# Performance work log

Measured on AMD Instinct MI355X. Metric: run time of the kernel, lower is better.

The kernel has to match this reference:

```python
import jax, jax.numpy as jnp
import numpy as np

NUM_HEADS = 12
NUM_TASKS = 4


def setup_inputs() -> dict:
    key = jax.random.key(0)
    k1, k2, k3, k4 = jax.random.split(key, 4)
    B, N, C = 2, 2048, 768
    x = jax.random.normal(k1, (B, N, C), dtype=jnp.float32)
    # nn.Linear(dim, 3*dim, bias=False): store as [C, 3C] so y = x @ w_qkv
    w_qkv = jax.random.normal(k2, (C, 3 * C), dtype=jnp.float32) * (C ** -0.5)
    w_proj = jax.random.normal(k3, (C, C), dtype=jnp.float32) * (C ** -0.5)
    b_proj = jax.random.normal(k4, (C,), dtype=jnp.float32) * 0.01
    return {"x": x, "w_qkv": w_qkv, "w_proj": w_proj, "b_proj": b_proj}


def reference(x, w_qkv, w_proj, b_proj):
    B, N, C = x.shape
    H = NUM_HEADS
    d = C // H
    scale = d ** -0.5
    qkv = (x @ w_qkv).reshape(B, N, 3, H, d)
    qkv = jnp.transpose(qkv, (2, 0, 3, 1, 4))  # [3, B, H, N, d]
    q, k, v = qkv[0], qkv[1], qkv[2]
    attn = jnp.einsum("bhnd,bhmd->bhnm", q, k) * scale
    attn = jax.nn.softmax(attn, axis=-1)
    # static task mask: zero cross-task attention among first NUM_TASKS tokens
    mask = jnp.ones((N, N), dtype=attn.dtype).at[:NUM_TASKS, :NUM_TASKS].set(
        jnp.eye(NUM_TASKS, dtype=attn.dtype))
    attn = attn * mask  # broadcasts over [B, H, N, N]
    out = jnp.einsum("bhnm,bhmd->bhnd", attn, v)
    out = jnp.transpose(out, (0, 2, 1, 3)).reshape(B, N, C)
    return out @ w_proj + b_proj
```

## Files before the change

### kernel.cpp

```cpp
#include <hip/hip_runtime.h>

typedef __attribute__((ext_vector_type(4))) float f32x4;
typedef __attribute__((ext_vector_type(8))) __bf16 bf16x8;
typedef __attribute__((ext_vector_type(4))) __bf16 bf16x4;

#define QSCALE (0.125f * 1.4426950408889634f)

__device__ __forceinline__ void load_lds16(const void* g, void* l) {
  __builtin_amdgcn_global_load_lds(
      (const __attribute__((address_space(1))) unsigned int*)g,
      (__attribute__((address_space(3))) unsigned int*)l, 16, 0, 0);
}

__device__ __forceinline__ f32x4 mfma16(bf16x8 a, bf16x8 b, f32x4 c) {
  return __builtin_amdgcn_mfma_f32_16x16x32_bf16(a, b, c, 0, 0, 0);
}

__device__ __forceinline__ bf16x8 cat44(bf16x4 a, bf16x4 b) {
  return __builtin_shufflevector(a, b, 0, 1, 2, 3, 4, 5, 6, 7);
}


__global__ __launch_bounds__(256) void k_cast_x(const float* __restrict__ in,
                                                __bf16* __restrict__ out) {
  int i = blockIdx.x * 256 + threadIdx.x;
  const f32x4* in4 = (const f32x4*)in;
  f32x4 a = in4[i * 2], b = in4[i * 2 + 1];
  bf16x8 o;
  o[0] = (__bf16)a[0]; o[1] = (__bf16)a[1]; o[2] = (__bf16)a[2]; o[3] = (__bf16)a[3];
  o[4] = (__bf16)b[0]; o[5] = (__bf16)b[1]; o[6] = (__bf16)b[2]; o[7] = (__bf16)b[3];
  *(bf16x8*)(out + (size_t)i * 8) = o;
}

__global__ void k_transpose_cast(const float* __restrict__ in, __bf16* __restrict__ out,
                                 int R, int C) {
  __shared__ float t[32][33];
  int c0 = blockIdx.x * 32, r0 = blockIdx.y * 32;
  int tx = threadIdx.x, ty = threadIdx.y;
#pragma unroll
  for (int j = 0; j < 32; j += 8)
    t[ty + j][tx] = in[(size_t)(r0 + ty + j) * C + c0 + tx];
  __syncthreads();
#pragma unroll
  for (int j = 0; j < 32; j += 8)
    out[(size_t)(c0 + ty + j) * R + r0 + tx] = (__bf16)t[tx][ty + j];
}


template <int NT>
__device__ __forceinline__ void gemm_core(const char* aB, const char* bB,
                                          char* smem, int tid, int l,
                                          int wr, int wc, f32x4 (&acc)[4][4]) {
  auto stage = [&](int buf, int kt) {
#pragma unroll
    for (int is = 0; is < 2; ++is) {
      int o = is * 4096 + tid * 16;
      int row = o >> 6, cb = (o >> 4) & 3;
      int src = row * 1536 + (((cb ^ row) & 3) << 4) + kt * 64;
      load_lds16(aB + src, smem + buf * 8192 + o);
      load_lds16(bB + src, smem + 16384 + buf * 8192 + o);
    }
  };
  stage(0, 0);
#pragma unroll 2
  for (int kt = 0; kt < NT; ++kt) {
    int cur = kt & 1;
    __syncthreads();
    if (kt + 1 < NT) stage(cur ^ 1, kt + 1);
    const __bf16* As = (const __bf16*)(smem + cur * 8192);
    const __bf16* Bs = (const __bf16*)(smem + 16384 + cur * 8192);
    bf16x8 af[4], bfr[4];
#pragma unroll
    for (int mf = 0; mf < 4; ++mf) {
      int row = wr * 64 + mf * 16 + (l & 15);
      af[mf] = *(const bf16x8*)&As[row * 32 + ((((l >> 4) ^ row) & 3) << 3)];
    }
#pragma unroll
    for (int nf = 0; nf < 4; ++nf) {
      int row = wc * 64 + nf * 16 + (l & 15);
      bfr[nf] = *(const bf16x8*)&Bs[row * 32 + ((((l >> 4) ^ row) & 3) << 3)];
    }
    __builtin_amdgcn_s_setprio(1);
#pragma unroll
    for (int mf = 0; mf < 4; ++mf)
#pragma unroll
      for (int nf = 0; nf < 4; ++nf)
        acc[mf][nf] = mfma16(af[mf], bfr[nf], acc[mf][nf]);
    __builtin_amdgcn_s_setprio(0);
  }
  __syncthreads();
}


__global__ __launch_bounds__(256, 3) void k_qkv(const __bf16* __restrict__ A,
                                                const __bf16* __restrict__ BT,
                                                __bf16* __restrict__ qb,
                                                __bf16* __restrict__ kb,
                                                __bf16* __restrict__ vT) {
  __shared__ __align__(16) char smem[32768];
  int tid = threadIdx.x, l = tid & 63, w = tid >> 6, wr = w >> 1, wc = w & 1;
  int g = l >> 4, c = l & 15;
  int m0 = blockIdx.y * 128, n0 = blockIdx.x * 128;
  f32x4 acc[4][4] = {};
  gemm_core<24>((const char*)(A + (size_t)m0 * 768), (const char*)(BT + (size_t)n0 * 768),
                smem, tid, l, wr, wc, acc);
  int b = m0 >> 11, m0l = m0 & 2047;
  int sel = n0 / 768;
  int rem = n0 - sel * 768;

  if (sel == 2) {
#pragma unroll
    for (int mf = 0; mf < 4; ++mf) {
      int tokb = wr * 64 + mf * 16 + 4 * g;
      int gr = tokb >> 3, low = (g & 1) << 3;
#pragma unroll
      for (int nf = 0; nf < 4; ++nf) {
        int dd = wc * 64 + nf * 16 + c;
        bf16x4 pk;
        pk[0] = (__bf16)acc[mf][nf][0]; pk[1] = (__bf16)acc[mf][nf][1];
        pk[2] = (__bf16)acc[mf][nf][2]; pk[3] = (__bf16)acc[mf][nf][3];
        *(bf16x4*)(smem + dd * 256 + (((gr ^ (dd & 15)) & 15) << 4) + low) = pk;
      }
    }
    __syncthreads();
#pragma unroll
    for (int p = 0; p < 8; ++p) {
      int idx = p * 256 + tid;
      int dd = idx >> 4, t8 = idx & 15;
      bf16x8 v = *(const bf16x8*)(smem + dd * 256 + (((t8 ^ (dd & 15)) & 15) << 4));
      int colg = rem + dd;
      int h = colg >> 6, d = colg & 63;
      *(bf16x8*)(vT + (((size_t)(b * 12 + h)) * 64 + d) * 2048 + m0l + t8 * 8) = v;
    }
  } else {
    float qs = (sel == 0) ? QSCALE : 1.0f;
#pragma unroll
    for (int mf = 0; mf < 4; ++mf)
#pragma unroll
      for (int nf = 0; nf < 4; ++nf) {
        int col = wc * 64 + nf * 16 + c;
        int grc = col >> 3, lowc = (col & 7) << 1;
#pragma unroll
        for (int r = 0; r < 4; ++r) {
          int tok = wr * 64 + mf * 16 + 4 * g + r;
          *(__bf16*)(smem + tok * 256 + (((grc ^ (tok & 15)) & 15) << 4) + lowc) =
              (__bf16)(acc[mf][nf][r] * qs);
        }
      }
    __syncthreads();
    __bf16* dst0 = (sel == 0) ? qb : kb;
#pragma unroll
    for (int p = 0; p < 8; ++p) {
      int idx = p * 256 + tid;
      int tok = idx >> 4, hh = (idx >> 3) & 1, d8 = idx & 7;
      int gr = hh * 8 + d8;
      bf16x8 v = *(const bf16x8*)(smem + tok * 256 + (((gr ^ (tok & 15)) & 15) << 4));
      int h = (rem >> 6) + hh;
      *(bf16x8*)(dst0 + (((size_t)(b * 12 + h)) * 2048 + m0l + tok) * 64 + d8 * 8) = v;
    }
  }
}


__global__ __launch_bounds__(256, 4) void k_attn(const __bf16* __restrict__ qb,
                                                 const __bf16* __restrict__ kb,
                                                 const __bf16* __restrict__ vT,
                                                 __bf16* __restrict__ Op01,
                                                 __bf16* __restrict__ Op23,
                                                 float* __restrict__ lpart) {
  __shared__ __align__(16) char smem[32768];
  int tid = threadIdx.x, l = tid & 63, w = tid >> 6;
  int g = l >> 4, c = l & 15;
  int phys = blockIdx.x;
  int lid = (phys & 7) * 192 + (phys >> 3);
  int qt = lid & 15;
  int bhsp = lid >> 4;
  int bh = bhsp % 24, sp = bhsp / 24;

  const char* qbase  = (const char*)qb + ((size_t)bh * 2048 + qt * 128) * 128;
  const char* kbase0 = (const char*)kb + (size_t)bh * 262144 + (size_t)sp * 65536;
  const char* vbase0 = (const char*)vT + (size_t)bh * 262144 + sp * 1024;

#pragma unroll
  for (int is = 0; is < 4; ++is) {
    int o = is * 4096 + tid * 16;
    int row = o >> 7, cb = (o >> 4) & 7;
    load_lds16(qbase + row * 128 + (((cb ^ row) & 7) << 4), smem + o);
  }
  __syncthreads();
  bf16x8 qf[2][2];
#pragma unroll
  for (int qi = 0; qi < 2; ++qi)
#pragma unroll
    for (int ks = 0; ks < 2; ++ks) {
      int q = w * 32 + qi * 16 + c;
      int gg = ks * 4 + g;
      qf[qi][ks] = *(const bf16x8*)(smem + q * 128 + (((gg ^ q) & 7) << 3) * 2);
    }
  __syncthreads();

  auto stageKV = [&](int buf, int t) {
    const char* kbase = kbase0 + t * 8192;
    const char* vbase = vbase0 + t * 128;
#pragma unroll
    for (int is = 0; is < 2; ++is) {
      int o = is * 4096 + tid * 16;
      int r = o >> 7, cb = (o >> 4) & 7;
      load_lds16(kbase + r * 128 + (((cb ^ r) & 7) << 4), smem + buf * 8192 + o);
      load_lds16(vbase + (size_t)r * 4096 + (((cb ^ r) & 7) << 4),
                 smem + 16384 + buf * 8192 + o);
    }
  };

  float lacc[2] = {0.f, 0.f};
  f32x4 accO[2][4] = {};

  stageKV(0, 0);
#pragma unroll 2
  for (int t = 0; t < 8; ++t) {
    int cur = t & 1;
    __syncthreads();
    if (t + 1 < 8) stageKV(cur ^ 1, t + 1);
    const char* KsB = smem + cur * 8192;
    const char* VsB = smem + 16384 + cur * 8192;

    f32x4 s[4][2];
#pragma unroll
    for (int kf = 0; kf < 4; ++kf) {
      s[kf][0] = f32x4{0.f, 0.f, 0.f, 0.f};
      s[kf][1] = f32x4{0.f, 0.f, 0.f, 0.f};
    }
    __builtin_amdgcn_s_setprio(1);
#pragma unroll
    for (int ks = 0; ks < 2; ++ks) {
#pragma unroll
      for (int kf = 0; kf < 4; ++kf) {
        int key = kf * 16 + c;
        int gg = ks * 4 + g;
        bf16x8 kfr = *(const bf16x8*)(KsB + key * 128 + (((gg ^ key) & 7) << 4));
        s[kf][0] = mfma16(kfr, qf[0][ks], s[kf][0]);
        s[kf][1] = mfma16(kfr, qf[1][ks], s[kf][1]);
      }
    }
    __builtin_amdgcn_s_setprio(0);

#pragma unroll
    for (int kf = 0; kf < 4; ++kf)
#pragma unroll
      for (int qi = 0; qi < 2; ++qi)
#pragma unroll
        for (int r = 0; r < 4; ++r) {
          float p = __builtin_amdgcn_exp2f(s[kf][qi][r]);
          s[kf][qi][r] = p;
          lacc[qi] += p;
        }

    if (sp == 0 && qt == 0 && t == 0 && w == 0 && g == 0 && c < 4) {
#pragma unroll
      for (int r = 0; r < 4; ++r)
        if (r != c) s[0][0][r] = 0.f;
    }

    bf16x4 pkv[2][4];
#pragma unroll
    for (int qi = 0; qi < 2; ++qi)
#pragma unroll
      for (int kf = 0; kf < 4; ++kf) {
        bf16x4 pk;
        pk[0] = (__bf16)s[kf][qi][0]; pk[1] = (__bf16)s[kf][qi][1];
        pk[2] = (__bf16)s[kf][qi][2]; pk[3] = (__bf16)s[kf][qi][3];
        pkv[qi][kf] = pk;
      }

    __builtin_amdgcn_s_setprio(1);
#pragma unroll
    for (int ks = 0; ks < 2; ++ks) {
      bf16x8 pa0 = cat44(pkv[0][2 * ks], pkv[0][2 * ks + 1]);
      bf16x8 pa1 = cat44(pkv[1][2 * ks], pkv[1][2 * ks + 1]);
      int low = (g & 1) << 3;
      int vc0 = ks * 4 + (g >> 1);
#pragma unroll
      for (int df = 0; df < 4; ++df) {
        int dd = df * 16 + c;
        const char* vrow = VsB + dd * 128;
        bf16x4 v0 = *(const bf16x4*)(vrow + (((vc0 ^ dd) & 7) << 4) + low);
        bf16x4 v1 = *(const bf16x4*)(vrow + ((((vc0 + 2) ^ dd) & 7) << 4) + low);
        bf16x8 vb = cat44(v0, v1);
        accO[0][df] = mfma16(pa0, vb, accO[0][df]);
        accO[1][df] = mfma16(pa1, vb, accO[1][df]);
      }
    }
    __builtin_amdgcn_s_setprio(0);
  }
  __syncthreads();

  size_t pbase = ((size_t)(sp & 1) * 24 + bh) * 2048 + qt * 128;
  __bf16* Obase = (sp < 2) ? Op01 : Op23;
  float lfull[2];
#pragma unroll
  for (int qi = 0; qi < 2; ++qi) {
    float rr = lacc[qi];
    rr += __shfl_xor(rr, 16, 64);
    rr += __shfl_xor(rr, 32, 64);
    lfull[qi] = rr;
  }
  if (g == 0) {
    size_t lb = ((size_t)sp * 24 + bh) * 2048 + qt * 128;
#pragma unroll
    for (int qi = 0; qi < 2; ++qi)
      lpart[lb + w * 32 + qi * 16 + c] = lfull[qi];
  }

  char* ep = smem + w * 4096;
#pragma unroll
  for (int mf = 0; mf < 2; ++mf) {
#pragma unroll
    for (int df = 0; df < 4; ++df) {
      int col = df * 16 + c;
      int sI = col >> 2, lowc = (col & 3) << 2;
#pragma unroll
      for (int r = 0; r < 4; ++r) {
        int rloc = 4 * g + r;
        *(float*)(ep + rloc * 256 + (((sI ^ rloc) & 15) << 4) + lowc) = accO[mf][df][r];
      }
    }
    int rr = l >> 2, q4 = l & 3;
    f32x4 aa[4];
#pragma unroll
    for (int j = 0; j < 4; ++j) {
      int sj = q4 * 4 + j;
      aa[j] = *(const f32x4*)(ep + rr * 256 + (((sj ^ rr) & 15) << 4));
    }
    bf16x8 o0, o1;
#pragma unroll
    for (int j = 0; j < 4; ++j) { o0[j] = (__bf16)aa[0][j]; o0[4 + j] = (__bf16)aa[1][j]; }
#pragma unroll
    for (int j = 0; j < 4; ++j) { o1[j] = (__bf16)aa[2][j]; o1[4 + j] = (__bf16)aa[3][j]; }
    int q = w * 32 + mf * 16 + rr;
    char* dst = (char*)Obase + (pbase + q) * 128 + q4 * 32;
    *(bf16x8*)dst = o0;
    *(bf16x8*)(dst + 16) = o1;
  }
}


__global__ __launch_bounds__(256) void k_combine(const __bf16* __restrict__ Op01,
                                                 const __bf16* __restrict__ Op23,
                                                 const float* __restrict__ lpart,
                                                 __bf16* __restrict__ ao) {
  int i = blockIdx.x * 256 + threadIdx.x;
  int d8 = i & 7, q = (i >> 3) & 2047, bh = i >> 14;
  int bg = bh / 12, h = bh - bg * 12;
  const size_t SPL = 24ull * 2048 * 64;
  size_t o0 = (((size_t)bh) * 2048 + q) * 64 + d8 * 8;
  bf16x8 a = *(const bf16x8*)(Op01 + o0);
  bf16x8 b = *(const bf16x8*)(Op01 + SPL + o0);
  bf16x8 cc = *(const bf16x8*)(Op23 + o0);
  bf16x8 d = *(const bf16x8*)(Op23 + SPL + o0);
  size_t lq = (size_t)bh * 2048 + q;
  float lsum = lpart[lq] + lpart[24ull * 2048 + lq] +
               lpart[2 * 24ull * 2048 + lq] + lpart[3 * 24ull * 2048 + lq];
  float rl = __builtin_amdgcn_rcpf(lsum);
  bf16x8 o;
#pragma unroll
  for (int j = 0; j < 8; ++j)
    o[j] = (__bf16)(((float)a[j] + (float)b[j] + (float)cc[j] + (float)d[j]) * rl);
  *(bf16x8*)(ao + ((size_t)bg * 2048 + q) * 768 + h * 64 + d8 * 8) = o;
}


__global__ __launch_bounds__(256, 3) void k_proj(const __bf16* __restrict__ A,
                                                 const __bf16* __restrict__ BT,
                                                 const float* __restrict__ bias,
                                                 float* __restrict__ out) {
  __shared__ __align__(16) char smem[32768];
  int tid = threadIdx.x, l = tid & 63, w = tid >> 6, wr = w >> 1, wc = w & 1;
  int m0 = blockIdx.y * 128, n0 = blockIdx.x * 128;
  f32x4 acc[4][4] = {};
  gemm_core<24>((const char*)(A + (size_t)m0 * 768), (const char*)(BT + (size_t)n0 * 768),
                smem, tid, l, wr, wc, acc);
#pragma unroll
  for (int nf = 0; nf < 4; ++nf) {
    int cc = n0 + wc * 64 + nf * 16 + (l & 15);
    float bi = bias[cc];
#pragma unroll
    for (int mf = 0; mf < 4; ++mf) {
      int m = m0 + wr * 64 + mf * 16 + ((l >> 4) << 2);
#pragma unroll
      for (int r = 0; r < 4; ++r)
        out[(size_t)(m + r) * 768 + cc] = acc[mf][nf][r] + bi;
    }
  }
}


extern "C" void kernel_launch(void* const* d_in, const int* in_sizes, int n_in,
                              void* d_out, int out_size, void* d_ws, size_t ws_size,
                              hipStream_t stream) {
  const float* x      = (const float*)d_in[0];
  const float* w_qkv  = (const float*)d_in[1];
  const float* w_proj = (const float*)d_in[2];
  const float* b_proj = (const float*)d_in[3];
  float* out = (float*)d_out;

  char* ws = (char*)d_ws;
  size_t off = 0;
  auto alloc = [&](size_t bytes) {
    char* p = ws + off;
    off += (bytes + 255) & ~(size_t)255;
    return p;
  };
  __bf16* xb     = (__bf16*)alloc(4096ull * 768 * 2);
  __bf16* wqkvT  = (__bf16*)alloc(2304ull * 768 * 2);
  __bf16* wprojT = (__bf16*)alloc(768ull * 768 * 2);
  __bf16* qb     = (__bf16*)alloc(24ull * 2048 * 64 * 2);
  __bf16* kb     = (__bf16*)alloc(24ull * 2048 * 64 * 2);
  __bf16* vT     = (__bf16*)alloc(24ull * 64 * 2048 * 2);
  __bf16* ao     = (__bf16*)alloc(4096ull * 768 * 2);
  __bf16* Op01   = (__bf16*)alloc(2ull * 24 * 2048 * 64 * 2);
  float*  lpart  = (float*)alloc(4ull * 24 * 2048 * 4);
  __bf16* Op23   = (__bf16*)d_out;

  k_cast_x<<<1536, 256, 0, stream>>>(x, xb);
  k_transpose_cast<<<dim3(72, 24), dim3(32, 8), 0, stream>>>(w_qkv, wqkvT, 768, 2304);
  k_transpose_cast<<<dim3(24, 24), dim3(32, 8), 0, stream>>>(w_proj, wprojT, 768, 768);
  k_qkv<<<dim3(18, 32), 256, 0, stream>>>(xb, wqkvT, qb, kb, vT);
  k_attn<<<1536, 256, 0, stream>>>(qb, kb, vT, Op01, Op23, lpart);
  k_combine<<<1536, 256, 0, stream>>>(Op01, Op23, lpart, ao);
  k_proj<<<dim3(6, 32), 256, 0, stream>>>(ao, wprojT, b_proj, out);
}
```

Baseline: 104.0 us.

## Triple-buffer GEMM and attention pipelines and halve attention KV split count

Replaces double-buffered LDS staging in the GEMM core and the attention kernel with a three-stage ring. Waits use explicit vmcnt waits plus raw barriers so two tiles stay in flight while one is computed. The attention split-K drops from 4 to 2 partitions, giving 768 blocks that each process 16 KV tiles, and the combine kernel now reads half the partial outputs. LDS per block grows to 48KB, which may reduce occupancy. Fewer attention blocks may also lower parallelism.

```diff
diff --git a/kernel.cpp b/kernel.cpp
--- a/kernel.cpp
+++ b/kernel.cpp
@@ -5,6 +5,13 @@
 typedef __attribute__((ext_vector_type(4))) __bf16 bf16x4;
 
 #define QSCALE (0.125f * 1.4426950408889634f)
+
+#define WAITV4 do { asm volatile("s_waitcnt vmcnt(4)" ::: "memory"); \
+  __builtin_amdgcn_sched_barrier(0); __builtin_amdgcn_s_barrier(); \
+  __builtin_amdgcn_sched_barrier(0); } while (0)
+#define WAITV0 do { asm volatile("s_waitcnt vmcnt(0)" ::: "memory"); \
+  __builtin_amdgcn_sched_barrier(0); __builtin_amdgcn_s_barrier(); \
+  __builtin_amdgcn_sched_barrier(0); } while (0)
 
 __device__ __forceinline__ void load_lds16(const void* g, void* l) {
   __builtin_amdgcn_global_load_lds(
@@ -47,10 +54,9 @@
 }
 
 
-template <int NT>
-__device__ __forceinline__ void gemm_core(const char* aB, const char* bB,
-                                          char* smem, int tid, int l,
-                                          int wr, int wc, f32x4 (&acc)[4][4]) {
+__device__ __forceinline__ void gemm_core24(const char* aB, const char* bB,
+                                            char* smem, int tid, int l,
+                                            int wr, int wc, f32x4 (&acc)[4][4]) {
   auto stage = [&](int buf, int kt) {
 #pragma unroll
     for (int is = 0; is < 2; ++is) {
@@ -58,17 +64,12 @@
       int row = o >> 6, cb = (o >> 4) & 3;
       int src = row * 1536 + (((cb ^ row) & 3) << 4) + kt * 64;
       load_lds16(aB + src, smem + buf * 8192 + o);
-      load_lds16(bB + src, smem + 16384 + buf * 8192 + o);
+      load_lds16(bB + src, smem + 24576 + buf * 8192 + o);
     }
   };
-  stage(0, 0);
-#pragma unroll 2
-  for (int kt = 0; kt < NT; ++kt) {
-    int cur = kt & 1;
-    __syncthreads();
-    if (kt + 1 < NT) stage(cur ^ 1, kt + 1);
-    const __bf16* As = (const __bf16*)(smem + cur * 8192);
-    const __bf16* Bs = (const __bf16*)(smem + 16384 + cur * 8192);
+  auto compute = [&](int buf) {
+    const __bf16* As = (const __bf16*)(smem + buf * 8192);
+    const __bf16* Bs = (const __bf16*)(smem + 24576 + buf * 8192);
     bf16x8 af[4], bfr[4];
 #pragma unroll
     for (int mf = 0; mf < 4; ++mf) {
@@ -87,7 +88,17 @@
       for (int nf = 0; nf < 4; ++nf)
         acc[mf][nf] = mfma16(af[mf], bfr[nf], acc[mf][nf]);
     __builtin_amdgcn_s_setprio(0);
-  }
+  };
+  stage(0, 0); stage(1, 1);
+#pragma unroll 3
+  for (int t = 0; t < 21; ++t) {
+    WAITV4;
+    stage((t + 2) % 3, t + 2);
+    compute(t % 3);
+  }
+  WAITV4; stage(2, 23); compute(0);
+  WAITV4; compute(1);
+  WAITV0; compute(2);
   __syncthreads();
 }
 
@@ -97,13 +108,13 @@
                                                 __bf16* __restrict__ qb,
                                                 __bf16* __restrict__ kb,
                                                 __bf16* __restrict__ vT) {
-  __shared__ __align__(16) char smem[32768];
+  __shared__ __align__(16) char smem[49152];
   int tid = threadIdx.x, l = tid & 63, w = tid >> 6, wr = w >> 1, wc = w & 1;
   int g = l >> 4, c = l & 15;
   int m0 = blockIdx.y * 128, n0 = blockIdx.x * 128;
   f32x4 acc[4][4] = {};
-  gemm_core<24>((const char*)(A + (size_t)m0 * 768), (const char*)(BT + (size_t)n0 * 768),
-                smem, tid, l, wr, wc, acc);
+  gemm_core24((const char*)(A + (size_t)m0 * 768), (const char*)(BT + (size_t)n0 * 768),
+              smem, tid, l, wr, wc, acc);
   int b = m0 >> 11, m0l = m0 & 2047;
   int sel = n0 / 768;
   int rem = n0 - sel * 768;
@@ -165,21 +176,20 @@
 __global__ __launch_bounds__(256, 4) void k_attn(const __bf16* __restrict__ qb,
                                                  const __bf16* __restrict__ kb,
                                                  const __bf16* __restrict__ vT,
-                                                 __bf16* __restrict__ Op01,
-                                                 __bf16* __restrict__ Op23,
+                                                 __bf16* __restrict__ Opart,
                                                  float* __restrict__ lpart) {
-  __shared__ __align__(16) char smem[32768];
+  __shared__ __align__(16) char smem[49152];
   int tid = threadIdx.x, l = tid & 63, w = tid >> 6;
   int g = l >> 4, c = l & 15;
   int phys = blockIdx.x;
-  int lid = (phys & 7) * 192 + (phys >> 3);
+  int lid = (phys & 7) * 96 + (phys >> 3);
   int qt = lid & 15;
   int bhsp = lid >> 4;
   int bh = bhsp % 24, sp = bhsp / 24;
 
   const char* qbase  = (const char*)qb + ((size_t)bh * 2048 + qt * 128) * 128;
-  const char* kbase0 = (const char*)kb + (size_t)bh * 262144 + (size_t)sp * 65536;
-  const char* vbase0 = (const char*)vT + (size_t)bh * 262144 + sp * 1024;
+  const char* kbase0 = (const char*)kb + (size_t)bh * 262144 + (size_t)sp * 131072;
+  const char* vbase0 = (const char*)vT + (size_t)bh * 262144 + sp * 2048;
 
 #pragma unroll
   for (int is = 0; is < 4; ++is) {
@@ -195,7 +205,7 @@
     for (int ks = 0; ks < 2; ++ks) {
       int q = w * 32 + qi * 16 + c;
       int gg = ks * 4 + g;
-      qf[qi][ks] = *(const bf16x8*)(smem + q * 128 + (((gg ^ q) & 7) << 3) * 2);
+      qf[qi][ks] = *(const bf16x8*)(smem + q * 128 + (((gg ^ q) & 7) << 4));
     }
   __syncthreads();
 
@@ -208,22 +218,16 @@
       int r = o >> 7, cb = (o >> 4) & 7;
       load_lds16(kbase + r * 128 + (((cb ^ r) & 7) << 4), smem + buf * 8192 + o);
       load_lds16(vbase + (size_t)r * 4096 + (((cb ^ r) & 7) << 4),
-                 smem + 16384 + buf * 8192 + o);
+                 smem + 24576 + buf * 8192 + o);
     }
   };
 
   float lacc[2] = {0.f, 0.f};
   f32x4 accO[2][4] = {};
 
-  stageKV(0, 0);
-#pragma unroll 2
-  for (int t = 0; t < 8; ++t) {
-    int cur = t & 1;
-    __syncthreads();
-    if (t + 1 < 8) stageKV(cur ^ 1, t + 1);
-    const char* KsB = smem + cur * 8192;
-    const char* VsB = smem + 16384 + cur * 8192;
-
+  auto compute = [&](int t, int buf) {
+    const char* KsB = smem + buf * 8192;
+    const char* VsB = smem + 24576 + buf * 8192;
     f32x4 s[4][2];
 #pragma unroll
     for (int kf = 0; kf < 4; ++kf) {
@@ -291,11 +295,22 @@
       }
     }
     __builtin_amdgcn_s_setprio(0);
-  }
+  };
+
+  stageKV(0, 0); stageKV(1, 1);
+#pragma unroll 3
+  for (int t = 0; t < 12; ++t) {
+    WAITV4;
+    stageKV((t + 2) % 3, t + 2);
+    compute(t, t % 3);
+  }
+  WAITV4; stageKV(2, 14); compute(12, 0);
+  WAITV4; stageKV(0, 15); compute(13, 1);
+  WAITV4; compute(14, 2);
+  WAITV0; compute(15, 0);
   __syncthreads();
 
-  size_t pbase = ((size_t)(sp & 1) * 24 + bh) * 2048 + qt * 128;
-  __bf16* Obase = (sp < 2) ? Op01 : Op23;
+  size_t pbase = ((size_t)sp * 24 + bh) * 2048 + qt * 128;
   float lfull[2];
 #pragma unroll
   for (int qi = 0; qi < 2; ++qi) {
@@ -305,10 +320,9 @@
     lfull[qi] = rr;
   }
   if (g == 0) {
-    size_t lb = ((size_t)sp * 24 + bh) * 2048 + qt * 128;
 #pragma unroll
     for (int qi = 0; qi < 2; ++qi)
-      lpart[lb + w * 32 + qi * 16 + c] = lfull[qi];
+      lpart[pbase + w * 32 + qi * 16 + c] = lfull[qi];
   }
 
   char* ep = smem + w * 4096;
@@ -324,6 +338,7 @@
         *(float*)(ep + rloc * 256 + (((sI ^ rloc) & 15) << 4) + lowc) = accO[mf][df][r];
       }
     }
+    asm volatile("s_waitcnt lgkmcnt(0)" ::: "memory");
     int rr = l >> 2, q4 = l & 3;
     f32x4 aa[4];
 #pragma unroll
@@ -337,15 +352,14 @@
 #pragma unroll
     for (int j = 0; j < 4; ++j) { o1[j] = (__bf16)aa[2][j]; o1[4 + j] = (__bf16)aa[3][j]; }
     int q = w * 32 + mf * 16 + rr;
-    char* dst = (char*)Obase + (pbase + q) * 128 + q4 * 32;
+    char* dst = (char*)Opart + (pbase + q) * 128 + q4 * 32;
     *(bf16x8*)dst = o0;
     *(bf16x8*)(dst + 16) = o1;
   }
 }
 
 
-__global__ __launch_bounds__(256) void k_combine(const __bf16* __restrict__ Op01,
-                                                 const __bf16* __restrict__ Op23,
+__global__ __launch_bounds__(256) void k_combine(const __bf16* __restrict__ Opart,
                                                  const float* __restrict__ lpart,
                                                  __bf16* __restrict__ ao) {
   int i = blockIdx.x * 256 + threadIdx.x;
@@ -353,18 +367,15 @@
   int bg = bh / 12, h = bh - bg * 12;
   const size_t SPL = 24ull * 2048 * 64;
   size_t o0 = (((size_t)bh) * 2048 + q) * 64 + d8 * 8;
-  bf16x8 a = *(const bf16x8*)(Op01 + o0);
-  bf16x8 b = *(const bf16x8*)(Op01 + SPL + o0);
-  bf16x8 cc = *(const bf16x8*)(Op23 + o0);
-  bf16x8 d = *(const bf16x8*)(Op23 + SPL + o0);
+  bf16x8 a = *(const bf16x8*)(Opart + o0);
+  bf16x8 b = *(const bf16x8*)(Opart + SPL + o0);
   size_t lq = (size_t)bh * 2048 + q;
-  float lsum = lpart[lq] + lpart[24ull * 2048 + lq] +
-               lpart[2 * 24ull * 2048 + lq] + lpart[3 * 24ull * 2048 + lq];
+  float lsum = lpart[lq] + lpart[24ull * 2048 + lq];
   float rl = __builtin_amdgcn_rcpf(lsum);
   bf16x8 o;
 #pragma unroll
   for (int j = 0; j < 8; ++j)
-    o[j] = (__bf16)(((float)a[j] + (float)b[j] + (float)cc[j] + (float)d[j]) * rl);
+    o[j] = (__bf16)(((float)a[j] + (float)b[j]) * rl);
   *(bf16x8*)(ao + ((size_t)bg * 2048 + q) * 768 + h * 64 + d8 * 8) = o;
 }
 
@@ -373,12 +384,12 @@
                                                  const __bf16* __restrict__ BT,
                                                  const float* __restrict__ bias,
                                                  float* __restrict__ out) {
-  __shared__ __align__(16) char smem[32768];
+  __shared__ __align__(16) char smem[49152];
   int tid = threadIdx.x, l = tid & 63, w = tid >> 6, wr = w >> 1, wc = w & 1;
   int m0 = blockIdx.y * 128, n0 = blockIdx.x * 128;
   f32x4 acc[4][4] = {};
-  gemm_core<24>((const char*)(A + (size_t)m0 * 768), (const char*)(BT + (size_t)n0 * 768),
-                smem, tid, l, wr, wc, acc);
+  gemm_core24((const char*)(A + (size_t)m0 * 768), (const char*)(BT + (size_t)n0 * 768),
+              smem, tid, l, wr, wc, acc);
 #pragma unroll
   for (int nf = 0; nf < 4; ++nf) {
     int cc = n0 + wc * 64 + nf * 16 + (l & 15);
@@ -417,15 +428,14 @@
   __bf16* kb     = (__bf16*)alloc(24ull * 2048 * 64 * 2);
   __bf16* vT     = (__bf16*)alloc(24ull * 64 * 2048 * 2);
   __bf16* ao     = (__bf16*)alloc(4096ull * 768 * 2);
-  __bf16* Op01   = (__bf16*)alloc(2ull * 24 * 2048 * 64 * 2);
-  float*  lpart  = (float*)alloc(4ull * 24 * 2048 * 4);
-  __bf16* Op23   = (__bf16*)d_out;
+  __bf16* Opart  = (__bf16*)alloc(2ull * 24 * 2048 * 64 * 2);
+  float*  lpart  = (float*)alloc(2ull * 24 * 2048 * 4);
 
   k_cast_x<<<1536, 256, 0, stream>>>(x, xb);
   k_transpose_cast<<<dim3(72, 24), dim3(32, 8), 0, stream>>>(w_qkv, wqkvT, 768, 2304);
   k_transpose_cast<<<dim3(24, 24), dim3(32, 8), 0, stream>>>(w_proj, wprojT, 768, 768);
   k_qkv<<<dim3(18, 32), 256, 0, stream>>>(xb, wqkvT, qb, kb, vT);
-  k_attn<<<1536, 256, 0, stream>>>(qb, kb, vT, Op01, Op23, lpart);
-  k_combine<<<1536, 256, 0, stream>>>(Op01, Op23, lpart, ao);
+  k_attn<<<768, 256, 0, stream>>>(qb, kb, vT, Opart, lpart);
+  k_combine<<<1536, 256, 0, stream>>>(Opart, lpart, ao);
   k_proj<<<dim3(6, 32), 256, 0, stream>>>(ao, wprojT, b_proj, out);
 }
```

Result: faster. 96.49 us (-7.2%).
